# Kernel tuning notes

Measured on AMD Instinct MI355X. Metric: run time of the kernel, lower is better.

## Reference

```python
import jax, jax.numpy as jnp
import numpy as np

C = 512
NUM_HEADS = 8
HEAD_DIM = C // NUM_HEADS  # 64
BN_EPS = 1e-5


def setup_inputs() -> dict:
    key = jax.random.key(0)
    ks = jax.random.split(key, 12)
    B, H, W = 8, 32, 32
    s = 0.02
    return {
        "x": jax.random.normal(ks[0], (B, C, H, W), dtype=jnp.float32),
        "gamma": jnp.ones((C,), jnp.float32),
        "beta": jnp.zeros((C,), jnp.float32),
        "rmean": jnp.zeros((C,), jnp.float32),
        "rvar": jnp.ones((C,), jnp.float32),
        "wq": jax.random.normal(ks[1], (C, C), jnp.float32) * s,
        "bq": jnp.zeros((C,), jnp.float32),
        "wk": jax.random.normal(ks[2], (C, C), jnp.float32) * s,
        "bk": jnp.zeros((C,), jnp.float32),
        "wv": jax.random.normal(ks[3], (C, C), jnp.float32) * s,
        "bv": jnp.zeros((C,), jnp.float32),
        "wp": jax.random.normal(ks[4], (C, C), jnp.float32) * s,
        "bp": jnp.zeros((C,), jnp.float32),
    }


def _conv1x1(w, b, h):
    # 1x1 conv == per-pixel dense: (O,C) x (B,C,H,W) -> (B,O,H,W)
    return jnp.einsum('oc,bchw->bohw', w, h) + b[None, :, None, None]


def reference(x, gamma, beta, rmean, rvar, wq, bq, wk, bk, wv, bv, wp, bp):
    B, Cc, H, W = x.shape
    N = H * W
    # BatchNorm2d (eval mode, running stats)
    inv = gamma / jnp.sqrt(rvar + BN_EPS)
    h = x * inv[None, :, None, None] + (beta - rmean * inv)[None, :, None, None]
    q = _conv1x1(wq, bq, h).reshape(B, NUM_HEADS, HEAD_DIM, N)
    k = _conv1x1(wk, bk, h).reshape(B, NUM_HEADS, HEAD_DIM, N)
    v = _conv1x1(wv, bv, h).reshape(B, NUM_HEADS, HEAD_DIM, N)
    scale = 1.0 / np.sqrt(HEAD_DIM).astype(np.float32)
    attn = jnp.einsum('bhdn,bhdm->bhnm', q, k) * scale  # [B,heads,N,N]
    attn = jnp.clip(attn, -50.0, 50.0)
    attn = jax.nn.softmax(attn, axis=-1)
    out = jnp.einsum('bhnm,bhdm->bhdn', attn, v).reshape(B, Cc, H, W)
    out = _conv1x1(wp, bp, out)
    return x + out
```

## Files before the change

kernel.cpp:

```cpp
#include <hip/hip_runtime.h>
#include <stdint.h>

#define C_DIM 512
#define NHEADS 8
#define HDIM 64
#define BATCH 8
#define NPIX 1024
#define Q_PRESCALE 0.18033688011112042f

typedef __bf16 bf16x8 __attribute__((ext_vector_type(8)));
typedef float f32x4 __attribute__((ext_vector_type(4)));
typedef float f32x16 __attribute__((ext_vector_type(16)));

__device__ __forceinline__ unsigned short f2bf(float f) {
  union { float f; unsigned u; } v; v.f = f;
  unsigned r = v.u + 0x7fffu + ((v.u >> 16) & 1u);
  return (unsigned short)(r >> 16);
}

__device__ __forceinline__ void gl_lds16(const void* g, void* l) {
  __builtin_amdgcn_global_load_lds(
      (__attribute__((address_space(1))) void*)g,
      (__attribute__((address_space(3))) void*)l,
      16, 0, 0);
}

__global__ __launch_bounds__(256) void k_prep(const float* __restrict__ wq,
                                              const float* __restrict__ wk,
                                              const float* __restrict__ wv,
                                              const float* __restrict__ wp,
                                              unsigned short* __restrict__ wbf) {
  const int n = C_DIM * C_DIM;
  for (int i = blockIdx.x * blockDim.x + threadIdx.x; i < 4 * n;
       i += gridDim.x * blockDim.x) {
    const float* src = (i < n) ? wq : (i < 2 * n) ? wk : (i < 3 * n) ? wv : wp;
    wbf[i] = f2bf(src[i & (n - 1)]);
  }
}

__global__ __launch_bounds__(256) void k_bnT(const float* __restrict__ x,
                                             const float* __restrict__ gamma,
                                             const float* __restrict__ beta,
                                             const float* __restrict__ rmean,
                                             const float* __restrict__ rvar,
                                             unsigned short* __restrict__ hbT) {
  __shared__ unsigned short tile[64][72];
  const int b = blockIdx.z, c0 = blockIdx.y * 64, n0 = blockIdx.x * 64;
  const int t = threadIdx.x;
#pragma unroll
  for (int it = 0; it < 4; ++it) {
    int c = it * 16 + (t >> 4);
    int n = (t & 15) * 4;
    const float4 v = *(const float4*)&x[((size_t)b * C_DIM + c0 + c) * NPIX + n0 + n];
    int cc = c0 + c;
    float inv = gamma[cc] * rsqrtf(rvar[cc] + 1e-5f);
    float add = beta[cc] - rmean[cc] * inv;
    tile[c][n + 0] = f2bf(v.x * inv + add);
    tile[c][n + 1] = f2bf(v.y * inv + add);
    tile[c][n + 2] = f2bf(v.z * inv + add);
    tile[c][n + 3] = f2bf(v.w * inv + add);
  }
  __syncthreads();
#pragma unroll
  for (int it = 0; it < 2; ++it) {
    int n = it * 32 + (t >> 3);
    int cj = (t & 7) * 8;
    unsigned short tmp[8];
#pragma unroll
    for (int u = 0; u < 8; ++u) tmp[u] = tile[cj + u][n];
    uint4 pk;
    pk.x = (unsigned)tmp[0] | ((unsigned)tmp[1] << 16);
    pk.y = (unsigned)tmp[2] | ((unsigned)tmp[3] << 16);
    pk.z = (unsigned)tmp[4] | ((unsigned)tmp[5] << 16);
    pk.w = (unsigned)tmp[6] | ((unsigned)tmp[7] << 16);
    *(uint4*)&hbT[((size_t)b * NPIX + n0 + n) * C_DIM + c0 + cj] = pk;
  }
}

__global__ __launch_bounds__(256) void k_qkv(const unsigned short* __restrict__ wbf,
                                             const float* __restrict__ bq,
                                             const float* __restrict__ bk,
                                             const float* __restrict__ bv,
                                             const unsigned short* __restrict__ hbT,
                                             unsigned short* __restrict__ QT,
                                             unsigned short* __restrict__ KT,
                                             unsigned short* __restrict__ Vb) {
  __shared__ unsigned short Atile[128 * 64];
  __shared__ unsigned short Btile[128 * 64];
  const int which = blockIdx.z >> 3;
  const int b = blockIdx.z & 7;
  const int m0 = blockIdx.y * 128, n0 = blockIdx.x * 128;
  const unsigned short* W = wbf + (size_t)which * C_DIM * C_DIM;
  const int t = threadIdx.x, wave = t >> 6, lane = t & 63;
  const int wr = wave >> 1, wc = wave & 1;
  f32x4 acc[4][4] = {};

  for (int k0 = 0; k0 < C_DIM; k0 += 64) {
    __syncthreads();
#pragma unroll
    for (int s = 0; s < 4; ++s) {
      int row = s * 32 + wave * 8 + (lane >> 3);
      int srcc = ((lane & 7) ^ (row & 7)) * 8;
      gl_lds16(&W[(size_t)(m0 + row) * C_DIM + k0 + srcc],
               &Atile[(s * 32 + wave * 8) * 64]);
      gl_lds16(&hbT[((size_t)b * NPIX + n0 + row) * C_DIM + k0 + srcc],
               &Btile[(s * 32 + wave * 8) * 64]);
    }
    __syncthreads();
#pragma unroll
    for (int ks2 = 0; ks2 < 2; ++ks2) {
      bf16x8 af[4], bfr[4];
#pragma unroll
      for (int i = 0; i < 4; ++i) {
        int row = wr * 64 + i * 16 + (lane & 15);
        int phys = (ks2 * 4 + (lane >> 4)) ^ (row & 7);
        af[i] = *(const bf16x8*)&Atile[row * 64 + phys * 8];
      }
#pragma unroll
      for (int j = 0; j < 4; ++j) {
        int row = wc * 64 + j * 16 + (lane & 15);
        int phys = (ks2 * 4 + (lane >> 4)) ^ (row & 7);
        bfr[j] = *(const bf16x8*)&Btile[row * 64 + phys * 8];
      }
#pragma unroll
      for (int i = 0; i < 4; ++i)
#pragma unroll
        for (int j = 0; j < 4; ++j)
          acc[i][j] = __builtin_amdgcn_mfma_f32_16x16x32_bf16(af[i], bfr[j], acc[i][j], 0, 0, 0);
    }
  }

  const float* bias = (which == 0) ? bq : (which == 1) ? bk : bv;
  if (which < 2) {
    unsigned short* T = (which == 0) ? QT : KT;
    const float qs = (which == 0) ? Q_PRESCALE : 1.0f;
#pragma unroll
    for (int i = 0; i < 4; ++i) {
      int o = m0 + wr * 64 + i * 16 + (lane >> 4) * 4;
      float b0 = bias[o + 0], b1 = bias[o + 1], b2 = bias[o + 2], b3 = bias[o + 3];
#pragma unroll
      for (int j = 0; j < 4; ++j) {
        int n = n0 + wc * 64 + j * 16 + (lane & 15);
        ushort4 pk;
        pk.x = f2bf((acc[i][j][0] + b0) * qs);
        pk.y = f2bf((acc[i][j][1] + b1) * qs);
        pk.z = f2bf((acc[i][j][2] + b2) * qs);
        pk.w = f2bf((acc[i][j][3] + b3) * qs);
        *(ushort4*)&T[((size_t)b * NPIX + n) * C_DIM + o] = pk;
      }
    }
  } else {
#pragma unroll
    for (int i = 0; i < 4; ++i) {
      int o = m0 + wr * 64 + i * 16 + (lane >> 4) * 4;
#pragma unroll
      for (int j = 0; j < 4; ++j) {
        int n = n0 + wc * 64 + j * 16 + (lane & 15);
#pragma unroll
        for (int r = 0; r < 4; ++r)
          Vb[((size_t)b * C_DIM + o + r) * NPIX + n] = f2bf(acc[i][j][r] + bias[o + r]);
      }
    }
  }
}

__global__ __launch_bounds__(512, 6) void k_attn(const unsigned short* __restrict__ QT,
                                                 const unsigned short* __restrict__ KT,
                                                 const unsigned short* __restrict__ Vb,
                                                 unsigned short* __restrict__ Opart,
                                                 float* __restrict__ rs) {
  __shared__ unsigned short Ks[2][64 * 64];
  __shared__ unsigned short Vs[2][64 * 64];
  __shared__ float rs_lds[256];

  const int bid = blockIdx.x;
  const int b = bid & 7, h = (bid >> 3) & 7, qt = (bid >> 6) & 3, ks = bid >> 8;
  const int n0 = qt * 256;
  const int kbase0 = ks * 512;
  const int lane = threadIdx.x & 63, wave = threadIdx.x >> 6;
  const int l31 = lane & 31, hi = lane >> 5;

  bf16x8 qf[4];
  {
    const unsigned short* qbase =
        QT + ((size_t)b * NPIX + n0 + wave * 32 + l31) * C_DIM + h * HDIM + hi * 8;
#pragma unroll
    for (int kk = 0; kk < 4; ++kk) qf[kk] = *(const bf16x8*)(qbase + kk * 16);
  }

  auto stage = [&](int buf, int tile) {
    const int m0 = kbase0 + tile * 64;
    int rb = wave * 8;
    int row = rb + (lane >> 3);
    int srcc = ((lane & 7) ^ (row & 7)) * 8;
    gl_lds16(&KT[((size_t)b * NPIX + m0 + row) * C_DIM + h * HDIM + srcc],
             &Ks[buf][rb * 64]);
    gl_lds16(&Vb[((size_t)b * C_DIM + h * HDIM + row) * NPIX + m0 + srcc],
             &Vs[buf][rb * 64]);
  };

  f32x16 oacc[2] = {};
  float rs0 = 0.f, rs1 = 0.f;

  stage(0, 0);
  __syncthreads();

  for (int tile = 0; tile < 8; ++tile) {
    const int cur = tile & 1;
    if (tile < 7) stage(cur ^ 1, tile + 1);

#pragma unroll
    for (int kt = 0; kt < 2; ++kt) {
      f32x16 s = {};
#pragma unroll
      for (int kk = 0; kk < 4; ++kk) {
        int row = kt * 32 + l31;
        int phys = (kk * 2 + hi) ^ (row & 7);
        bf16x8 kf = *(const bf16x8*)&Ks[cur][row * 64 + phys * 8];
        s = __builtin_amdgcn_mfma_f32_32x32x16_bf16(kf, qf[kk], s, 0, 0, 0);
      }
      unsigned w[8];
#pragma unroll
      for (int r2 = 0; r2 < 8; ++r2) {
        float e0 = exp2f(s[2 * r2]);
        float e1 = exp2f(s[2 * r2 + 1]);
        rs0 += e0;
        rs1 += e1;
        asm("v_cvt_pk_bf16_f32 %0, %1, %2" : "=v"(w[r2]) : "v"(e0), "v"(e1));
      }
      asm volatile("v_permlane32_swap_b32 %0, %1" : "+v"(w[0]), "+v"(w[2]));
      asm volatile("v_permlane32_swap_b32 %0, %1" : "+v"(w[1]), "+v"(w[3]));
      asm volatile("v_permlane32_swap_b32 %0, %1" : "+v"(w[4]), "+v"(w[6]));
      asm volatile("v_permlane32_swap_b32 %0, %1" : "+v"(w[5]), "+v"(w[7]));
      union U8 { unsigned u[4]; bf16x8 v; };
      U8 pa0, pa1;
      pa0.u[0] = w[0]; pa0.u[1] = w[1]; pa0.u[2] = w[2]; pa0.u[3] = w[3];
      pa1.u[0] = w[4]; pa1.u[1] = w[5]; pa1.u[2] = w[6]; pa1.u[3] = w[7];
#pragma unroll
      for (int dt = 0; dt < 2; ++dt) {
        int d = dt * 32 + l31;
        bf16x8 v0 = *(const bf16x8*)&Vs[cur][d * 64 + (((kt * 4 + hi) ^ (d & 7)) * 8)];
        bf16x8 v1 = *(const bf16x8*)&Vs[cur][d * 64 + (((kt * 4 + 2 + hi) ^ (d & 7)) * 8)];
        oacc[dt] = __builtin_amdgcn_mfma_f32_32x32x16_bf16(pa0.v, v0, oacc[dt], 0, 0, 0);
        oacc[dt] = __builtin_amdgcn_mfma_f32_32x32x16_bf16(pa1.v, v1, oacc[dt], 0, 0, 0);
      }
    }
    __syncthreads();
  }

  float rsq = rs0 + rs1;
  rsq += __shfl_xor(rsq, 32);
  if (hi == 0) rs_lds[wave * 32 + l31] = rsq;
  __syncthreads();

  float inv[16];
#pragma unroll
  for (int r = 0; r < 16; ++r)
    inv[r] = 1.0f / rs_lds[wave * 32 + (r & 3) + 8 * (r >> 2) + 4 * hi];

  __bf16* obase = (__bf16*)(Opart + (size_t)ks * BATCH * NPIX * C_DIM +
                            ((size_t)b * NPIX + n0 + wave * 32) * C_DIM +
                            h * HDIM + l31);
#pragma unroll
  for (int dt = 0; dt < 2; ++dt)
#pragma unroll
    for (int r = 0; r < 16; ++r) {
      int q = (r & 3) + 8 * (r >> 2) + 4 * hi;
      obase[(size_t)q * C_DIM + dt * 32] = (__bf16)(oacc[dt][r] * inv[r]);
    }
  if (hi == 0)
    rs[(((size_t)ks * 8 + b) * 8 + h) * NPIX + n0 + wave * 32 + l31] = rsq;
}

__global__ __launch_bounds__(256) void k_comb(const unsigned short* OA,
                                              const unsigned short* OB,
                                              const float* __restrict__ rs,
                                              unsigned short* AOT) {
  int i = blockIdx.x * 256 + threadIdx.x;
  int b = i >> 16;
  int rem = i & 65535;
  int n = rem >> 6;
  int c8 = rem & 63;
  int h = c8 >> 3;
  size_t off = ((size_t)b * NPIX + n) * C_DIM + c8 * 8;
  float rsA = rs[(((size_t)0 * 8 + b) * 8 + h) * NPIX + n];
  float rsB = rs[(((size_t)1 * 8 + b) * 8 + h) * NPIX + n];
  float sA = rsA / (rsA + rsB);
  float sB = 1.0f - sA;
  uint4 a = *(const uint4*)(OA + off);
  uint4 bb = *(const uint4*)(OB + off);
  const unsigned* au = (const unsigned*)&a;
  const unsigned* bu = (const unsigned*)&bb;
  uint4 o;
  unsigned* ou = (unsigned*)&o;
#pragma unroll
  for (int j = 0; j < 4; ++j) {
    float a0, a1, b0, b1;
    union { unsigned u; float f; } t;
    t.u = (au[j] & 0xFFFFu) << 16; a0 = t.f;
    t.u = au[j] & 0xFFFF0000u;     a1 = t.f;
    t.u = (bu[j] & 0xFFFFu) << 16; b0 = t.f;
    t.u = bu[j] & 0xFFFF0000u;     b1 = t.f;
    float o0 = sA * a0 + sB * b0;
    float o1 = sA * a1 + sB * b1;
    unsigned pk;
    asm("v_cvt_pk_bf16_f32 %0, %1, %2" : "=v"(pk) : "v"(o0), "v"(o1));
    ou[j] = pk;
  }
  *(uint4*)(AOT + off) = o;
}

__global__ __launch_bounds__(256) void k_proj(const unsigned short* __restrict__ Wp,
                                              const float* __restrict__ bp,
                                              const unsigned short* __restrict__ AOT,
                                              const float* __restrict__ x,
                                              float* __restrict__ out) {
  __shared__ unsigned short Atile[128 * 32];
  __shared__ unsigned short Btile[128 * 32];
  const int b = blockIdx.z;
  const int m0 = blockIdx.y * 128, n0 = blockIdx.x * 128;
  const int t = threadIdx.x, wave = t >> 6, lane = t & 63;
  const int wr = wave >> 1, wc = wave & 1;
  f32x4 acc[4][4] = {};
  const int st_row = lane >> 2;
  const int st_col = (((lane & 3) ^ ((lane >> 3) & 3))) * 8;

  for (int k0 = 0; k0 < C_DIM; k0 += 32) {
    __syncthreads();
#pragma unroll
    for (int it = 0; it < 2; ++it) {
      int q = wave + 4 * it;
      int row = q * 16 + st_row;
      gl_lds16(&Wp[(size_t)(m0 + row) * C_DIM + k0 + st_col], &Atile[q * 512]);
      gl_lds16(&AOT[((size_t)b * NPIX + n0 + row) * C_DIM + k0 + st_col], &Btile[q * 512]);
    }
    __syncthreads();
    bf16x8 af[4], bfr[4];
#pragma unroll
    for (int i = 0; i < 4; ++i) {
      int row = wr * 64 + i * 16 + (lane & 15);
      af[i] = *(const bf16x8*)&Atile[row * 32 + (((lane >> 4) ^ ((row >> 1) & 3)) * 8)];
    }
#pragma unroll
    for (int j = 0; j < 4; ++j) {
      int row = wc * 64 + j * 16 + (lane & 15);
      bfr[j] = *(const bf16x8*)&Btile[row * 32 + (((lane >> 4) ^ ((row >> 1) & 3)) * 8)];
    }
#pragma unroll
    for (int i = 0; i < 4; ++i)
#pragma unroll
      for (int j = 0; j < 4; ++j)
        acc[i][j] = __builtin_amdgcn_mfma_f32_16x16x32_bf16(af[i], bfr[j], acc[i][j], 0, 0, 0);
  }

#pragma unroll
  for (int i = 0; i < 4; ++i) {
    int o = m0 + wr * 64 + i * 16 + (lane >> 4) * 4;
    float b0 = bp[o + 0], b1 = bp[o + 1], b2 = bp[o + 2], b3 = bp[o + 3];
#pragma unroll
    for (int j = 0; j < 4; ++j) {
      int n = n0 + wc * 64 + j * 16 + (lane & 15);
      size_t base = ((size_t)b * C_DIM + o) * NPIX + n;
      out[base + 0 * NPIX] = acc[i][j][0] + b0 + x[base + 0 * NPIX];
      out[base + 1 * NPIX] = acc[i][j][1] + b1 + x[base + 1 * NPIX];
      out[base + 2 * NPIX] = acc[i][j][2] + b2 + x[base + 2 * NPIX];
      out[base + 3 * NPIX] = acc[i][j][3] + b3 + x[base + 3 * NPIX];
    }
  }
}

extern "C" void kernel_launch(void* const* d_in, const int* in_sizes, int n_in,
                              void* d_out, int out_size, void* d_ws, size_t ws_size,
                              hipStream_t stream) {
  (void)in_sizes; (void)n_in; (void)out_size; (void)ws_size;
  const float* x     = (const float*)d_in[0];
  const float* gamma = (const float*)d_in[1];
  const float* beta  = (const float*)d_in[2];
  const float* rmean = (const float*)d_in[3];
  const float* rvar  = (const float*)d_in[4];
  const float* wq    = (const float*)d_in[5];
  const float* bq    = (const float*)d_in[6];
  const float* wk    = (const float*)d_in[7];
  const float* bk    = (const float*)d_in[8];
  const float* wv    = (const float*)d_in[9];
  const float* bv    = (const float*)d_in[10];
  const float* wp    = (const float*)d_in[11];
  const float* bp    = (const float*)d_in[12];

  unsigned short* ws  = (unsigned short*)d_ws;
  const size_t WSZ    = (size_t)C_DIM * C_DIM;
  const size_t BIG    = (size_t)BATCH * NPIX * C_DIM;
  unsigned short* wbf   = ws;
  unsigned short* hbT   = wbf + 4 * WSZ;
  unsigned short* QT    = hbT + BIG;
  unsigned short* KT    = QT + BIG;
  unsigned short* Vb    = KT + BIG;
  unsigned short* AOT   = Vb + BIG;
  unsigned short* Opart = AOT + BIG;
  float*          rs    = (float*)(Opart + 2 * BIG);

  k_prep<<<dim3(512), dim3(256), 0, stream>>>(wq, wk, wv, wp, wbf);
  k_bnT<<<dim3(16, 8, 8), dim3(256), 0, stream>>>(x, gamma, beta, rmean, rvar, hbT);
  k_qkv<<<dim3(8, 4, 24), dim3(256), 0, stream>>>(wbf, bq, bk, bv, hbT, QT, KT, Vb);
  k_attn<<<dim3(512), dim3(512), 0, stream>>>(QT, KT, Vb, Opart, rs);
  k_comb<<<dim3(2048), dim3(256), 0, stream>>>(Opart, Opart + BIG, rs, AOT);
  k_proj<<<dim3(8, 4, 8), dim3(256), 0, stream>>>(wbf + 3 * WSZ, bp, AOT, x, (float*)d_out);
}
```

Baseline: 203.7 us.

## Fuse split-K attention combine into projection and shrink attention blocks

Removes the separate combine kernel by merging the two partial attention outputs, weighted by their row sums, directly while the projection GEMM loads its B tiles into LDS. The attention kernel now uses 256-thread blocks covering 128 queries, doubling the grid to 1024 blocks, with each wave staging two row groups of K/V. Output store loops are reordered. This drops one kernel launch and the intermediate buffer round trip. In exchange, projection tile loads become synchronous register loads instead of direct-to-LDS async copies, and the partial outputs are re-read by every M-tile block.

```diff
diff --git a/kernel.cpp b/kernel.cpp
--- a/kernel.cpp
+++ b/kernel.cpp
@@ -164,18 +164,18 @@
   }
 }
 
-__global__ __launch_bounds__(512, 6) void k_attn(const unsigned short* __restrict__ QT,
-                                                 const unsigned short* __restrict__ KT,
-                                                 const unsigned short* __restrict__ Vb,
-                                                 unsigned short* __restrict__ Opart,
-                                                 float* __restrict__ rs) {
+__global__ __launch_bounds__(256) void k_attn(const unsigned short* __restrict__ QT,
+                                              const unsigned short* __restrict__ KT,
+                                              const unsigned short* __restrict__ Vb,
+                                              unsigned short* __restrict__ Opart,
+                                              float* __restrict__ rs) {
   __shared__ unsigned short Ks[2][64 * 64];
   __shared__ unsigned short Vs[2][64 * 64];
-  __shared__ float rs_lds[256];
+  __shared__ float rs_lds[128];
 
   const int bid = blockIdx.x;
-  const int b = bid & 7, h = (bid >> 3) & 7, qt = (bid >> 6) & 3, ks = bid >> 8;
-  const int n0 = qt * 256;
+  const int b = bid & 7, h = (bid >> 3) & 7, qt = (bid >> 6) & 7, ks = bid >> 9;
+  const int n0 = qt * 128;
   const int kbase0 = ks * 512;
   const int lane = threadIdx.x & 63, wave = threadIdx.x >> 6;
   const int l31 = lane & 31, hi = lane >> 5;
@@ -190,13 +190,16 @@
 
   auto stage = [&](int buf, int tile) {
     const int m0 = kbase0 + tile * 64;
-    int rb = wave * 8;
-    int row = rb + (lane >> 3);
-    int srcc = ((lane & 7) ^ (row & 7)) * 8;
-    gl_lds16(&KT[((size_t)b * NPIX + m0 + row) * C_DIM + h * HDIM + srcc],
-             &Ks[buf][rb * 64]);
-    gl_lds16(&Vb[((size_t)b * C_DIM + h * HDIM + row) * NPIX + m0 + srcc],
-             &Vs[buf][rb * 64]);
+#pragma unroll
+    for (int it = 0; it < 2; ++it) {
+      int rb = it * 32 + wave * 8;
+      int row = rb + (lane >> 3);
+      int srcc = ((lane & 7) ^ (row & 7)) * 8;
+      gl_lds16(&KT[((size_t)b * NPIX + m0 + row) * C_DIM + h * HDIM + srcc],
+               &Ks[buf][rb * 64]);
+      gl_lds16(&Vb[((size_t)b * C_DIM + h * HDIM + row) * NPIX + m0 + srcc],
+               &Vs[buf][rb * 64]);
+    }
   };
 
   f32x16 oacc[2] = {};
@@ -262,57 +265,21 @@
                             ((size_t)b * NPIX + n0 + wave * 32) * C_DIM +
                             h * HDIM + l31);
 #pragma unroll
-  for (int dt = 0; dt < 2; ++dt)
-#pragma unroll
-    for (int r = 0; r < 16; ++r) {
-      int q = (r & 3) + 8 * (r >> 2) + 4 * hi;
+  for (int r = 0; r < 16; ++r) {
+    int q = (r & 3) + 8 * (r >> 2) + 4 * hi;
+#pragma unroll
+    for (int dt = 0; dt < 2; ++dt)
       obase[(size_t)q * C_DIM + dt * 32] = (__bf16)(oacc[dt][r] * inv[r]);
-    }
+  }
   if (hi == 0)
     rs[(((size_t)ks * 8 + b) * 8 + h) * NPIX + n0 + wave * 32 + l31] = rsq;
 }
 
-__global__ __launch_bounds__(256) void k_comb(const unsigned short* OA,
-                                              const unsigned short* OB,
-                                              const float* __restrict__ rs,
-                                              unsigned short* AOT) {
-  int i = blockIdx.x * 256 + threadIdx.x;
-  int b = i >> 16;
-  int rem = i & 65535;
-  int n = rem >> 6;
-  int c8 = rem & 63;
-  int h = c8 >> 3;
-  size_t off = ((size_t)b * NPIX + n) * C_DIM + c8 * 8;
-  float rsA = rs[(((size_t)0 * 8 + b) * 8 + h) * NPIX + n];
-  float rsB = rs[(((size_t)1 * 8 + b) * 8 + h) * NPIX + n];
-  float sA = rsA / (rsA + rsB);
-  float sB = 1.0f - sA;
-  uint4 a = *(const uint4*)(OA + off);
-  uint4 bb = *(const uint4*)(OB + off);
-  const unsigned* au = (const unsigned*)&a;
-  const unsigned* bu = (const unsigned*)&bb;
-  uint4 o;
-  unsigned* ou = (unsigned*)&o;
-#pragma unroll
-  for (int j = 0; j < 4; ++j) {
-    float a0, a1, b0, b1;
-    union { unsigned u; float f; } t;
-    t.u = (au[j] & 0xFFFFu) << 16; a0 = t.f;
-    t.u = au[j] & 0xFFFF0000u;     a1 = t.f;
-    t.u = (bu[j] & 0xFFFFu) << 16; b0 = t.f;
-    t.u = bu[j] & 0xFFFF0000u;     b1 = t.f;
-    float o0 = sA * a0 + sB * b0;
-    float o1 = sA * a1 + sB * b1;
-    unsigned pk;
-    asm("v_cvt_pk_bf16_f32 %0, %1, %2" : "=v"(pk) : "v"(o0), "v"(o1));
-    ou[j] = pk;
-  }
-  *(uint4*)(AOT + off) = o;
-}
-
 __global__ __launch_bounds__(256) void k_proj(const unsigned short* __restrict__ Wp,
                                               const float* __restrict__ bp,
-                                              const unsigned short* __restrict__ AOT,
+                                              const unsigned short* __restrict__ OpA,
+                                              const unsigned short* __restrict__ OpB,
+                                              const float* __restrict__ rs,
                                               const float* __restrict__ x,
                                               float* __restrict__ out) {
   __shared__ unsigned short Atile[128 * 32];
@@ -327,12 +294,39 @@
 
   for (int k0 = 0; k0 < C_DIM; k0 += 32) {
     __syncthreads();
+    const int hh = (k0 + st_col) >> 6;
 #pragma unroll
     for (int it = 0; it < 2; ++it) {
       int q = wave + 4 * it;
       int row = q * 16 + st_row;
       gl_lds16(&Wp[(size_t)(m0 + row) * C_DIM + k0 + st_col], &Atile[q * 512]);
-      gl_lds16(&AOT[((size_t)b * NPIX + n0 + row) * C_DIM + k0 + st_col], &Btile[q * 512]);
+      int n = n0 + row;
+      float rsA = rs[((size_t)(0 * 8 + b) * 8 + hh) * NPIX + n];
+      float rsB = rs[((size_t)(1 * 8 + b) * 8 + hh) * NPIX + n];
+      float sA = rsA / (rsA + rsB);
+      float sB = 1.0f - sA;
+      size_t off = ((size_t)b * NPIX + n) * C_DIM + k0 + st_col;
+      uint4 ua = *(const uint4*)(OpA + off);
+      uint4 ub = *(const uint4*)(OpB + off);
+      const unsigned* au = (const unsigned*)&ua;
+      const unsigned* bu = (const unsigned*)&ub;
+      uint4 o;
+      unsigned* ou = (unsigned*)&o;
+#pragma unroll
+      for (int j = 0; j < 4; ++j) {
+        union { unsigned u; float f; } tt;
+        float a0, a1, b0, b1;
+        tt.u = (au[j] & 0xFFFFu) << 16; a0 = tt.f;
+        tt.u = au[j] & 0xFFFF0000u;     a1 = tt.f;
+        tt.u = (bu[j] & 0xFFFFu) << 16; b0 = tt.f;
+        tt.u = bu[j] & 0xFFFF0000u;     b1 = tt.f;
+        float o0 = sA * a0 + sB * b0;
+        float o1 = sA * a1 + sB * b1;
+        unsigned pk;
+        asm("v_cvt_pk_bf16_f32 %0, %1, %2" : "=v"(pk) : "v"(o0), "v"(o1));
+        ou[j] = pk;
+      }
+      *(uint4*)&Btile[q * 512 + lane * 8] = o;
     }
     __syncthreads();
     bf16x8 af[4], bfr[4];
@@ -395,14 +389,12 @@
   unsigned short* QT    = hbT + BIG;
   unsigned short* KT    = QT + BIG;
   unsigned short* Vb    = KT + BIG;
-  unsigned short* AOT   = Vb + BIG;
-  unsigned short* Opart = AOT + BIG;
+  unsigned short* Opart = Vb + BIG;
   float*          rs    = (float*)(Opart + 2 * BIG);
 
   k_prep<<<dim3(512), dim3(256), 0, stream>>>(wq, wk, wv, wp, wbf);
   k_bnT<<<dim3(16, 8, 8), dim3(256), 0, stream>>>(x, gamma, beta, rmean, rvar, hbT);
   k_qkv<<<dim3(8, 4, 24), dim3(256), 0, stream>>>(wbf, bq, bk, bv, hbT, QT, KT, Vb);
-  k_attn<<<dim3(512), dim3(512), 0, stream>>>(QT, KT, Vb, Opart, rs);
-  k_comb<<<dim3(2048), dim3(256), 0, stream>>>(Opart, Opart + BIG, rs, AOT);
-  k_proj<<<dim3(8, 4, 8), dim3(256), 0, stream>>>(wbf + 3 * WSZ, bp, AOT, x, (float*)d_out);
-}
+  k_attn<<<dim3(1024), dim3(256), 0, stream>>>(QT, KT, Vb, Opart, rs);
+  k_proj<<<dim3(8, 4, 8), dim3(256), 0, stream>>>(wbf + 3 * WSZ, bp, Opart, Opart + BIG, rs, x, (float*)d_out);
+}
```

Measured after the change: 179.4 us. -11.9%, faster.

## Fuse Q/K/V projections per block and shrink attention blocks to 256 threads

Applied to the files above, without the earlier changes.

The QKV GEMM now computes all three projections in one block. It stages a 64-row slice of each weight matrix against one shared 128-pixel activation tile, so the activation tile is loaded from memory once instead of three times. The attention kernel moves from 512-thread blocks over 256 queries to 256-thread blocks over 128 queries, doubling the block count, and each thread now stages two K/V rows. The workspace layout is also reshuffled, with AOT placed after rs. The trade-offs are more accumulator registers in the QKV kernel and more K/V tile loads across the larger number of attention blocks.

```diff
diff --git a/kernel.cpp b/kernel.cpp
--- a/kernel.cpp
+++ b/kernel.cpp
@@ -85,97 +85,114 @@
                                              unsigned short* __restrict__ QT,
                                              unsigned short* __restrict__ KT,
                                              unsigned short* __restrict__ Vb) {
-  __shared__ unsigned short Atile[128 * 64];
-  __shared__ unsigned short Btile[128 * 64];
-  const int which = blockIdx.z >> 3;
-  const int b = blockIdx.z & 7;
-  const int m0 = blockIdx.y * 128, n0 = blockIdx.x * 128;
-  const unsigned short* W = wbf + (size_t)which * C_DIM * C_DIM;
+  __shared__ unsigned short At[3][64 * 64];
+  __shared__ unsigned short Bt[128 * 64];
+  const int b = blockIdx.z;
+  const int m0 = blockIdx.y * 64, n0 = blockIdx.x * 128;
   const int t = threadIdx.x, wave = t >> 6, lane = t & 63;
   const int wr = wave >> 1, wc = wave & 1;
-  f32x4 acc[4][4] = {};
+  f32x4 acc[3][2][4] = {};
+
+  const int row8 = wave * 8 + (lane >> 3);
 
   for (int k0 = 0; k0 < C_DIM; k0 += 64) {
     __syncthreads();
 #pragma unroll
+    for (int w3 = 0; w3 < 3; ++w3) {
+      const unsigned short* W = wbf + (size_t)w3 * (C_DIM * C_DIM);
+#pragma unroll
+      for (int s = 0; s < 2; ++s) {
+        int row = s * 32 + row8;
+        int sc = ((lane & 7) ^ (row & 7)) * 8;
+        gl_lds16(&W[(size_t)(m0 + row) * C_DIM + k0 + sc],
+                 &At[w3][(s * 32 + wave * 8) * 64]);
+      }
+    }
+#pragma unroll
     for (int s = 0; s < 4; ++s) {
-      int row = s * 32 + wave * 8 + (lane >> 3);
-      int srcc = ((lane & 7) ^ (row & 7)) * 8;
-      gl_lds16(&W[(size_t)(m0 + row) * C_DIM + k0 + srcc],
-               &Atile[(s * 32 + wave * 8) * 64]);
-      gl_lds16(&hbT[((size_t)b * NPIX + n0 + row) * C_DIM + k0 + srcc],
-               &Btile[(s * 32 + wave * 8) * 64]);
+      int row = s * 32 + row8;
+      int sc = ((lane & 7) ^ (row & 7)) * 8;
+      gl_lds16(&hbT[((size_t)b * NPIX + n0 + row) * C_DIM + k0 + sc],
+               &Bt[(s * 32 + wave * 8) * 64]);
     }
     __syncthreads();
 #pragma unroll
     for (int ks2 = 0; ks2 < 2; ++ks2) {
-      bf16x8 af[4], bfr[4];
-#pragma unroll
-      for (int i = 0; i < 4; ++i) {
-        int row = wr * 64 + i * 16 + (lane & 15);
-        int phys = (ks2 * 4 + (lane >> 4)) ^ (row & 7);
-        af[i] = *(const bf16x8*)&Atile[row * 64 + phys * 8];
-      }
+      bf16x8 bfr[4];
 #pragma unroll
       for (int j = 0; j < 4; ++j) {
         int row = wc * 64 + j * 16 + (lane & 15);
         int phys = (ks2 * 4 + (lane >> 4)) ^ (row & 7);
-        bfr[j] = *(const bf16x8*)&Btile[row * 64 + phys * 8];
-      }
-#pragma unroll
-      for (int i = 0; i < 4; ++i)
-#pragma unroll
-        for (int j = 0; j < 4; ++j)
-          acc[i][j] = __builtin_amdgcn_mfma_f32_16x16x32_bf16(af[i], bfr[j], acc[i][j], 0, 0, 0);
-    }
-  }
-
-  const float* bias = (which == 0) ? bq : (which == 1) ? bk : bv;
-  if (which < 2) {
-    unsigned short* T = (which == 0) ? QT : KT;
-    const float qs = (which == 0) ? Q_PRESCALE : 1.0f;
-#pragma unroll
-    for (int i = 0; i < 4; ++i) {
-      int o = m0 + wr * 64 + i * 16 + (lane >> 4) * 4;
-      float b0 = bias[o + 0], b1 = bias[o + 1], b2 = bias[o + 2], b3 = bias[o + 3];
-#pragma unroll
-      for (int j = 0; j < 4; ++j) {
-        int n = n0 + wc * 64 + j * 16 + (lane & 15);
-        ushort4 pk;
-        pk.x = f2bf((acc[i][j][0] + b0) * qs);
-        pk.y = f2bf((acc[i][j][1] + b1) * qs);
-        pk.z = f2bf((acc[i][j][2] + b2) * qs);
-        pk.w = f2bf((acc[i][j][3] + b3) * qs);
-        *(ushort4*)&T[((size_t)b * NPIX + n) * C_DIM + o] = pk;
-      }
-    }
-  } else {
-#pragma unroll
-    for (int i = 0; i < 4; ++i) {
-      int o = m0 + wr * 64 + i * 16 + (lane >> 4) * 4;
-#pragma unroll
-      for (int j = 0; j < 4; ++j) {
-        int n = n0 + wc * 64 + j * 16 + (lane & 15);
-#pragma unroll
-        for (int r = 0; r < 4; ++r)
-          Vb[((size_t)b * C_DIM + o + r) * NPIX + n] = f2bf(acc[i][j][r] + bias[o + r]);
-      }
-    }
-  }
-}
-
-__global__ __launch_bounds__(512, 6) void k_attn(const unsigned short* __restrict__ QT,
-                                                 const unsigned short* __restrict__ KT,
-                                                 const unsigned short* __restrict__ Vb,
-                                                 unsigned short* __restrict__ Opart,
-                                                 float* __restrict__ rs) {
+        bfr[j] = *(const bf16x8*)&Bt[row * 64 + phys * 8];
+      }
+#pragma unroll
+      for (int w3 = 0; w3 < 3; ++w3) {
+        bf16x8 af[2];
+#pragma unroll
+        for (int i = 0; i < 2; ++i) {
+          int row = wr * 32 + i * 16 + (lane & 15);
+          int phys = (ks2 * 4 + (lane >> 4)) ^ (row & 7);
+          af[i] = *(const bf16x8*)&At[w3][row * 64 + phys * 8];
+        }
+#pragma unroll
+        for (int i = 0; i < 2; ++i)
+#pragma unroll
+          for (int j = 0; j < 4; ++j)
+            acc[w3][i][j] = __builtin_amdgcn_mfma_f32_16x16x32_bf16(
+                af[i], bfr[j], acc[w3][i][j], 0, 0, 0);
+      }
+    }
+  }
+
+#pragma unroll
+  for (int w3 = 0; w3 < 3; ++w3) {
+    const float* bias = (w3 == 0) ? bq : (w3 == 1) ? bk : bv;
+    if (w3 < 2) {
+      unsigned short* T = (w3 == 0) ? QT : KT;
+      const float qs = (w3 == 0) ? Q_PRESCALE : 1.0f;
+#pragma unroll
+      for (int i = 0; i < 2; ++i) {
+        int o = m0 + wr * 32 + i * 16 + (lane >> 4) * 4;
+        float b0 = bias[o + 0], b1 = bias[o + 1], b2 = bias[o + 2], b3 = bias[o + 3];
+#pragma unroll
+        for (int j = 0; j < 4; ++j) {
+          int n = n0 + wc * 64 + j * 16 + (lane & 15);
+          ushort4 pk;
+          pk.x = f2bf((acc[w3][i][j][0] + b0) * qs);
+          pk.y = f2bf((acc[w3][i][j][1] + b1) * qs);
+          pk.z = f2bf((acc[w3][i][j][2] + b2) * qs);
+          pk.w = f2bf((acc[w3][i][j][3] + b3) * qs);
+          *(ushort4*)&T[((size_t)b * NPIX + n) * C_DIM + o] = pk;
+        }
+      }
+    } else {
+#pragma unroll
+      for (int i = 0; i < 2; ++i) {
+        int o = m0 + wr * 32 + i * 16 + (lane >> 4) * 4;
+#pragma unroll
+        for (int j = 0; j < 4; ++j) {
+          int n = n0 + wc * 64 + j * 16 + (lane & 15);
+#pragma unroll
+          for (int r = 0; r < 4; ++r)
+            Vb[((size_t)b * C_DIM + o + r) * NPIX + n] = f2bf(acc[w3][i][j][r] + bias[o + r]);
+        }
+      }
+    }
+  }
+}
+
+__global__ __launch_bounds__(256) void k_attn(const unsigned short* __restrict__ QT,
+                                              const unsigned short* __restrict__ KT,
+                                              const unsigned short* __restrict__ Vb,
+                                              unsigned short* __restrict__ Opart,
+                                              float* __restrict__ rs) {
   __shared__ unsigned short Ks[2][64 * 64];
   __shared__ unsigned short Vs[2][64 * 64];
-  __shared__ float rs_lds[256];
+  __shared__ float rs_lds[128];
 
   const int bid = blockIdx.x;
-  const int b = bid & 7, h = (bid >> 3) & 7, qt = (bid >> 6) & 3, ks = bid >> 8;
-  const int n0 = qt * 256;
+  const int b = bid & 7, h = (bid >> 3) & 7, qt = (bid >> 6) & 7, ks = bid >> 9;
+  const int n0 = qt * 128;
   const int kbase0 = ks * 512;
   const int lane = threadIdx.x & 63, wave = threadIdx.x >> 6;
   const int l31 = lane & 31, hi = lane >> 5;
@@ -190,13 +207,16 @@
 
   auto stage = [&](int buf, int tile) {
     const int m0 = kbase0 + tile * 64;
-    int rb = wave * 8;
-    int row = rb + (lane >> 3);
-    int srcc = ((lane & 7) ^ (row & 7)) * 8;
-    gl_lds16(&KT[((size_t)b * NPIX + m0 + row) * C_DIM + h * HDIM + srcc],
-             &Ks[buf][rb * 64]);
-    gl_lds16(&Vb[((size_t)b * C_DIM + h * HDIM + row) * NPIX + m0 + srcc],
-             &Vs[buf][rb * 64]);
+#pragma unroll
+    for (int it = 0; it < 2; ++it) {
+      int rb = it * 32 + wave * 8;
+      int row = rb + (lane >> 3);
+      int srcc = ((lane & 7) ^ (row & 7)) * 8;
+      gl_lds16(&KT[((size_t)b * NPIX + m0 + row) * C_DIM + h * HDIM + srcc],
+               &Ks[buf][rb * 64]);
+      gl_lds16(&Vb[((size_t)b * C_DIM + h * HDIM + row) * NPIX + m0 + srcc],
+               &Vs[buf][rb * 64]);
+    }
   };
 
   f32x16 oacc[2] = {};
@@ -262,12 +282,12 @@
                             ((size_t)b * NPIX + n0 + wave * 32) * C_DIM +
                             h * HDIM + l31);
 #pragma unroll
-  for (int dt = 0; dt < 2; ++dt)
-#pragma unroll
-    for (int r = 0; r < 16; ++r) {
-      int q = (r & 3) + 8 * (r >> 2) + 4 * hi;
+  for (int r = 0; r < 16; ++r) {
+    int q = (r & 3) + 8 * (r >> 2) + 4 * hi;
+#pragma unroll
+    for (int dt = 0; dt < 2; ++dt)
       obase[(size_t)q * C_DIM + dt * 32] = (__bf16)(oacc[dt][r] * inv[r]);
-    }
+  }
   if (hi == 0)
     rs[(((size_t)ks * 8 + b) * 8 + h) * NPIX + n0 + wave * 32 + l31] = rsq;
 }
@@ -395,14 +415,14 @@
   unsigned short* QT    = hbT + BIG;
   unsigned short* KT    = QT + BIG;
   unsigned short* Vb    = KT + BIG;
-  unsigned short* AOT   = Vb + BIG;
-  unsigned short* Opart = AOT + BIG;
+  unsigned short* Opart = Vb + BIG;
   float*          rs    = (float*)(Opart + 2 * BIG);
+  unsigned short* AOT   = (unsigned short*)(rs + 2 * 8 * 8 * 1024);
 
   k_prep<<<dim3(512), dim3(256), 0, stream>>>(wq, wk, wv, wp, wbf);
   k_bnT<<<dim3(16, 8, 8), dim3(256), 0, stream>>>(x, gamma, beta, rmean, rvar, hbT);
-  k_qkv<<<dim3(8, 4, 24), dim3(256), 0, stream>>>(wbf, bq, bk, bv, hbT, QT, KT, Vb);
-  k_attn<<<dim3(512), dim3(512), 0, stream>>>(QT, KT, Vb, Opart, rs);
+  k_qkv<<<dim3(8, 8, 8), dim3(256), 0, stream>>>(wbf, bq, bk, bv, hbT, QT, KT, Vb);
+  k_attn<<<dim3(1024), dim3(256), 0, stream>>>(QT, KT, Vb, Opart, rs);
   k_comb<<<dim3(2048), dim3(256), 0, stream>>>(Opart, Opart + BIG, rs, AOT);
   k_proj<<<dim3(8, 4, 8), dim3(256), 0, stream>>>(wbf + 3 * WSZ, bp, AOT, x, (float*)d_out);
 }
```

Result: faster. 177.9 us (-12.7%).
